# Kernel optimization log

Measured on AMD Instinct MI355X. Metric: run time of the kernel, lower is better.

## Reference

```python
import jax, jax.numpy as jnp
import numpy as np

EMBED_DIM = 1024
NUM_HEADS = 16
HEAD_DIM = EMBED_DIM // NUM_HEADS
SCALE = HEAD_DIM ** -0.5


def setup_inputs() -> dict:
    key = jax.random.key(0)
    ks = jax.random.split(key, 5)
    B, S = 4, 2048
    x = jax.random.normal(ks[0], (B, S, EMBED_DIM), dtype=jnp.float32)
    # Dense(embed_dim*3): kernel [D, 3D], bias [3D] (Keras glorot_uniform; use scaled normal)
    w_qkv = jax.random.normal(ks[1], (EMBED_DIM, 3 * EMBED_DIM), dtype=jnp.float32) * (1.0 / np.sqrt(EMBED_DIM))
    b_qkv = jnp.zeros((3 * EMBED_DIM,), dtype=jnp.float32)
    w_proj = jax.random.normal(ks[2], (EMBED_DIM, EMBED_DIM), dtype=jnp.float32) * (1.0 / np.sqrt(EMBED_DIM))
    b_proj = jnp.zeros((EMBED_DIM,), dtype=jnp.float32)
    return {"x": x, "w_qkv": w_qkv, "b_qkv": b_qkv, "w_proj": w_proj, "b_proj": b_proj}


def reference(x, w_qkv, b_qkv, w_proj, b_proj):
    B, S, D = x.shape
    qkv = x @ w_qkv + b_qkv
    qkv = qkv.reshape(B, S, 3, NUM_HEADS, HEAD_DIM)
    qkv = jnp.transpose(qkv, (2, 0, 3, 1, 4))
    q, k, v = qkv[0], qkv[1], qkv[2]
    # scaled dot-product attention (full [B,H,S,S] scores, matching source)
    attn_logits = jnp.einsum('bhqd,bhkd->bhqk', q, k) * SCALE
    attn = jax.nn.softmax(attn_logits, axis=-1)
    context = jnp.einsum('bhqk,bhkd->bhqd', attn, v)
    context = jnp.transpose(context, (0, 2, 1, 3)).reshape(B, S, D)
    out = context @ w_proj + b_proj
    return out
```

## Files before the change

### kernel.cpp

```cpp
#include <hip/hip_runtime.h>

typedef unsigned short u16;
typedef __attribute__((ext_vector_type(8))) short bf16x8;
typedef __attribute__((ext_vector_type(4))) float f32x4;
typedef __attribute__((ext_vector_type(16))) float f32x16;

__device__ __forceinline__ float bf2f(u16 x) {
  union { unsigned u; float f; } v; v.u = ((unsigned)x) << 16; return v.f;
}
__device__ __forceinline__ u16 f2bf(float f) {
  union { float f; unsigned u; } v; v.f = f;
  unsigned r = v.u + 0x7FFFu + ((v.u >> 16) & 1u);
  return (u16)(r >> 16);
}
__device__ __forceinline__ float clampf(float v) {
  return fmaxf(fminf(v, 1.0e4f), -1.0e4f);
}
__device__ __forceinline__ void gll16(const u16* g, u16* l) {
  __builtin_amdgcn_global_load_lds(
      (const __attribute__((address_space(1))) void*)g,
      (__attribute__((address_space(3))) void*)l, 16, 0, 0);
}
__device__ __forceinline__ unsigned cvtpk(float lo, float hi) {
  unsigned r;
  asm("v_cvt_pk_bf16_f32 %0, %1, %2" : "=v"(r) : "v"(lo), "v"(hi));
  return r;
}

__global__ __launch_bounds__(256) void convert_x(
    const float* __restrict__ x, u16* __restrict__ xbf) {
  const int i0 = (blockIdx.x * 256 + threadIdx.x) * 4;
  const float4 v = *(const float4*)(x + i0);
  xbf[i0 + 0] = f2bf(v.x); xbf[i0 + 1] = f2bf(v.y);
  xbf[i0 + 2] = f2bf(v.z); xbf[i0 + 3] = f2bf(v.w);
}

__global__ __launch_bounds__(256) void transpose_f32_bf16(
    const float* __restrict__ in, u16* __restrict__ out, int R, int C) {
  __shared__ u16 tile[32][33];
  const int bc = blockIdx.x * 32, br = blockIdx.y * 32;
  const int tx = threadIdx.x & 31, ty = threadIdx.x >> 5;
  #pragma unroll
  for (int i = ty; i < 32; i += 8)
    tile[i][tx] = f2bf(in[(size_t)(br + i) * C + bc + tx]);
  __syncthreads();
  #pragma unroll
  for (int i = ty; i < 32; i += 8)
    out[(size_t)(bc + i) * R + br + tx] = tile[tx][i];
}

__global__ __launch_bounds__(256) void gemm1_qkv(
    const u16* __restrict__ A, const u16* __restrict__ Bt,
    const float* __restrict__ bias, u16* __restrict__ qk,
    u16* __restrict__ vt, int K) {
  __shared__ u16 As0[128 * 32], As1[128 * 32];
  __shared__ u16 Bs0[128 * 32], Bs1[128 * 32];
  const int tid = threadIdx.x;
  const int m0 = blockIdx.x * 128, n0 = blockIdx.y * 128;
  const int wave = tid >> 6, lane = tid & 63;
  const int quad = lane >> 4, l16 = lane & 15;
  const int wm = (wave >> 1) * 64, wn = (wave & 1) * 64;
  const int sr = (lane >> 2), sp = lane & 3;

  f32x4 acc[4][4] = {};
  const u16* gA = A + (size_t)(m0 + wave * 32 + sr) * K + sp * 8;
  const u16* gB = Bt + (size_t)(n0 + wave * 32 + sr) * K + sp * 8;

  for (int k0 = 0; k0 < K; k0 += 64) {
    #pragma unroll
    for (int t = 0; t < 2; ++t) {
      gll16(gA + (size_t)(t * 16) * K + k0,      &As0[(wave * 32 + t * 16) * 32]);
      gll16(gA + (size_t)(t * 16) * K + k0 + 32, &As1[(wave * 32 + t * 16) * 32]);
      gll16(gB + (size_t)(t * 16) * K + k0,      &Bs0[(wave * 32 + t * 16) * 32]);
      gll16(gB + (size_t)(t * 16) * K + k0 + 32, &Bs1[(wave * 32 + t * 16) * 32]);
    }
    __syncthreads();
    #pragma unroll
    for (int ks = 0; ks < 2; ++ks) {
      const u16* Ah = ks ? As1 : As0;
      const u16* Bh = ks ? Bs1 : Bs0;
      bf16x8 af[4], bfr[4];
      #pragma unroll
      for (int i = 0; i < 4; ++i)
        af[i] = *(const bf16x8*)&Ah[(wm + i * 16 + l16) * 32 + quad * 8];
      #pragma unroll
      for (int j = 0; j < 4; ++j)
        bfr[j] = *(const bf16x8*)&Bh[(wn + j * 16 + l16) * 32 + quad * 8];
      #pragma unroll
      for (int i = 0; i < 4; ++i)
        #pragma unroll
        for (int j = 0; j < 4; ++j)
          acc[i][j] = __builtin_amdgcn_mfma_f32_16x16x32_bf16(af[i], bfr[j], acc[i][j], 0, 0, 0);
    }
    __syncthreads();
  }

  #pragma unroll
  for (int i = 0; i < 4; ++i) {
    const int row = m0 + wm + i * 16 + quad * 4;
    #pragma unroll
    for (int j = 0; j < 4; ++j) {
      const int col = n0 + wn + j * 16 + l16;
      const float bv = bias[col];
      if (col < 2048) {
        #pragma unroll
        for (int r = 0; r < 4; ++r)
          qk[(size_t)(row + r) * 2048 + col] = f2bf(clampf(acc[i][j][r] + bv));
      } else {
        const int d = col & 63;
        const int hh = (col - 2048) >> 6;
        #pragma unroll
        for (int r = 0; r < 4; ++r) {
          const int rr = row + r;
          const int bb = rr >> 11, ss = rr & 2047;
          vt[(size_t)(bb * 16 + hh) * 131072 + d * 2048 + ss] =
              f2bf(clampf(acc[i][j][r] + bv));
        }
      }
    }
  }
}

__global__ __launch_bounds__(256) void gemm2_proj(
    const u16* __restrict__ A, const u16* __restrict__ Bt,
    const float* __restrict__ bias, float* __restrict__ out, int K) {
  __shared__ u16 As0[128 * 32], As1[128 * 32];
  __shared__ u16 Bs0[128 * 32], Bs1[128 * 32];
  const int tid = threadIdx.x;
  const int m0 = blockIdx.x * 128, n0 = blockIdx.y * 128;
  const int wave = tid >> 6, lane = tid & 63;
  const int quad = lane >> 4, l16 = lane & 15;
  const int wm = (wave >> 1) * 64, wn = (wave & 1) * 64;
  const int sr = (lane >> 2), sp = lane & 3;

  f32x4 acc[4][4] = {};
  const u16* gA = A + (size_t)(m0 + wave * 32 + sr) * K + sp * 8;
  const u16* gB = Bt + (size_t)(n0 + wave * 32 + sr) * K + sp * 8;

  for (int k0 = 0; k0 < K; k0 += 64) {
    #pragma unroll
    for (int t = 0; t < 2; ++t) {
      gll16(gA + (size_t)(t * 16) * K + k0,      &As0[(wave * 32 + t * 16) * 32]);
      gll16(gA + (size_t)(t * 16) * K + k0 + 32, &As1[(wave * 32 + t * 16) * 32]);
      gll16(gB + (size_t)(t * 16) * K + k0,      &Bs0[(wave * 32 + t * 16) * 32]);
      gll16(gB + (size_t)(t * 16) * K + k0 + 32, &Bs1[(wave * 32 + t * 16) * 32]);
    }
    __syncthreads();
    #pragma unroll
    for (int ks = 0; ks < 2; ++ks) {
      const u16* Ah = ks ? As1 : As0;
      const u16* Bh = ks ? Bs1 : Bs0;
      bf16x8 af[4], bfr[4];
      #pragma unroll
      for (int i = 0; i < 4; ++i)
        af[i] = *(const bf16x8*)&Ah[(wm + i * 16 + l16) * 32 + quad * 8];
      #pragma unroll
      for (int j = 0; j < 4; ++j)
        bfr[j] = *(const bf16x8*)&Bh[(wn + j * 16 + l16) * 32 + quad * 8];
      #pragma unroll
      for (int i = 0; i < 4; ++i)
        #pragma unroll
        for (int j = 0; j < 4; ++j)
          acc[i][j] = __builtin_amdgcn_mfma_f32_16x16x32_bf16(af[i], bfr[j], acc[i][j], 0, 0, 0);
    }
    __syncthreads();
  }

  #pragma unroll
  for (int i = 0; i < 4; ++i) {
    const int row = m0 + wm + i * 16 + quad * 4;
    #pragma unroll
    for (int j = 0; j < 4; ++j) {
      const int col = n0 + wn + j * 16 + l16;
      const float bv = bias[col];
      #pragma unroll
      for (int r = 0; r < 4; ++r)
        out[(size_t)(row + r) * 1024 + col] = clampf(acc[i][j][r] + bv);
    }
  }
}

__device__ __forceinline__ int swz(int row, int col) {
  const int key = (row ^ (row >> 2)) & 7;
  return row * 64 + (((col >> 3) ^ key) << 3) + (col & 7);
}

__global__ __launch_bounds__(256, 4) void attn_fused(
    const u16* __restrict__ qk, const u16* __restrict__ vt,
    u16* __restrict__ ctx) {
  __shared__ u16 Ks[64 * 64];
  __shared__ u16 VsT[64 * 64];
  __shared__ u16 big[10240];
  const int bh = blockIdx.x, qt = blockIdx.y;
  const int b = bh >> 4, h = bh & 15;
  const int tid = threadIdx.x;
  const int w = tid >> 6, lane = tid & 63;
  const int l31 = lane & 31, hl = lane >> 5;
  const int qbase = qt * 128 + w * 32;
  const int xaddr = (lane ^ 32) << 2;

  const u16* qptr = qk + (size_t)(b * 2048) * 2048 + h * 64;
  bf16x8 qf[4];
  #pragma unroll
  for (int ds = 0; ds < 4; ++ds)
    qf[ds] = *(const bf16x8*)(qptr + (size_t)(qbase + l31) * 2048 + ds * 16 + hl * 8);

  const u16* kptr = qk + (size_t)(b * 2048) * 2048 + 1024 + h * 64;
  const u16* vptr = vt + (size_t)bh * 131072;

  const int srow = tid >> 3, scol = (tid & 7) * 8;

  const int st0 = swz(srow, scol);
  const int st1 = swz(srow + 32, scol);
  int off[2][4];
  #pragma unroll
  for (int a = 0; a < 2; ++a)
    #pragma unroll
    for (int d = 0; d < 4; ++d)
      off[a][d] = swz(a * 32 + l31, d * 16 + hl * 8);

  const u16* kB0 = kptr + (size_t)srow * 2048 + scol;
  const u16* kB1 = kptr + (size_t)(srow + 32) * 2048 + scol;
  const u16* vB0 = vptr + (size_t)srow * 2048 + scol;
  const u16* vB1 = vptr + (size_t)(srow + 32) * 2048 + scol;

  f32x16 o[2] = {};
  float lacc = 0.0f;
  const float c2 = 0.125f * 1.44269504088896340736f;

  bf16x8 k0 = *(const bf16x8*)kB0;
  bf16x8 k1 = *(const bf16x8*)kB1;
  bf16x8 v0 = *(const bf16x8*)vB0;
  bf16x8 v1 = *(const bf16x8*)vB1;

  for (int kv0 = 0; kv0 < 2048; kv0 += 64) {
    __syncthreads();
    *(bf16x8*)&Ks[st0]  = k0;
    *(bf16x8*)&Ks[st1]  = k1;
    *(bf16x8*)&VsT[st0] = v0;
    *(bf16x8*)&VsT[st1] = v1;
    __syncthreads();
    const int kvn = (kv0 + 64) & 2047;
    k0 = *(const bf16x8*)(kB0 + (size_t)kvn * 2048);
    k1 = *(const bf16x8*)(kB1 + (size_t)kvn * 2048);
    v0 = *(const bf16x8*)(vB0 + kvn);
    v1 = *(const bf16x8*)(vB1 + kvn);

    #pragma unroll
    for (int kb = 0; kb < 2; ++kb) {
      f32x16 s = {};
      #pragma unroll
      for (int ds = 0; ds < 4; ++ds) {
        bf16x8 kf = *(const bf16x8*)&Ks[off[kb][ds]];
        s = __builtin_amdgcn_mfma_f32_32x32x16_bf16(kf, qf[ds], s, 0, 0, 0);
      }
      #pragma unroll
      for (int r = 0; r < 16; ++r)
        s[r] = __builtin_amdgcn_exp2f(s[r] * c2);
      {
        float t0 = (s[0] + s[1]) + (s[2] + s[3]);
        float t1 = (s[4] + s[5]) + (s[6] + s[7]);
        float t2 = (s[8] + s[9]) + (s[10] + s[11]);
        float t3 = (s[12] + s[13]) + (s[14] + s[15]);
        lacc += (t0 + t1) + (t2 + t3);
      }
      #pragma unroll
      for (int ksl = 0; ksl < 2; ++ksl) {
        const int r0 = ksl * 8;
        unsigned cA = cvtpk(s[r0 + 0], s[r0 + 1]);
        unsigned cB = cvtpk(s[r0 + 2], s[r0 + 3]);
        unsigned cC = cvtpk(s[r0 + 4], s[r0 + 5]);
        unsigned cD = cvtpk(s[r0 + 6], s[r0 + 7]);
        const unsigned bA = (unsigned)__builtin_amdgcn_ds_bpermute(xaddr, (int)cA);
        const unsigned bB = (unsigned)__builtin_amdgcn_ds_bpermute(xaddr, (int)cB);
        const unsigned bC = (unsigned)__builtin_amdgcn_ds_bpermute(xaddr, (int)cC);
        const unsigned bD = (unsigned)__builtin_amdgcn_ds_bpermute(xaddr, (int)cD);
        union { unsigned u[4]; bf16x8 v; } pf;
        pf.u[0] = hl ? bC : cA;
        pf.u[1] = hl ? bD : cB;
        pf.u[2] = hl ? cC : bA;
        pf.u[3] = hl ? cD : bB;
        const int kg = kb * 2 + ksl;
        #pragma unroll
        for (int db = 0; db < 2; ++db) {
          bf16x8 vf = *(const bf16x8*)&VsT[off[db][kg]];
          o[db] = __builtin_amdgcn_mfma_f32_32x32x16_bf16(pf.v, vf, o[db], 0, 0, 0);
        }
      }
    }
  }

  {
    union { float f; int i; } a, rr;
    a.f = lacc;
    rr.i = __builtin_amdgcn_ds_bpermute(xaddr, a.i);
    lacc = lacc + rr.f;
  }
  float* dnm = (float*)big;
  if (lane < 32) dnm[w * 32 + lane] = lacc;
  u16* cbase = ctx + (size_t)(b * 2048) * 1024 + h * 64;
  #pragma unroll
  for (int r = 0; r < 16; ++r) {
    const int q0 = (r & 3) + 8 * (r >> 2) + 4 * hl;
    const float inv = 1.0f / dnm[w * 32 + q0];
    const size_t qrow = (size_t)(qbase + q0);
    cbase[qrow * 1024 + l31]      = f2bf(o[0][r] * inv);
    cbase[qrow * 1024 + 32 + l31] = f2bf(o[1][r] * inv);
  }
}

extern "C" void kernel_launch(void* const* d_in, const int* in_sizes, int n_in,
                              void* d_out, int out_size, void* d_ws, size_t ws_size,
                              hipStream_t stream) {
  (void)out_size;
  const float *x = nullptr, *wq = nullptr, *bq = nullptr, *wp = nullptr, *bp = nullptr;
  for (int i = 0; i < n_in; ++i) {
    switch (in_sizes[i]) {
      case 8388608: x  = (const float*)d_in[i]; break;
      case 3145728: wq = (const float*)d_in[i]; break;
      case 3072:    bq = (const float*)d_in[i]; break;
      case 1048576: wp = (const float*)d_in[i]; break;
      case 1024:    bp = (const float*)d_in[i]; break;
      default: break;
    }
  }
  if (!x || !wq || !bq || !wp || !bp) {
    x  = (const float*)d_in[0]; wq = (const float*)d_in[1];
    bq = (const float*)d_in[2]; wp = (const float*)d_in[3];
    bp = (const float*)d_in[4];
  }
  float* out = (float*)d_out;

  const size_t NEED = 75497472;
  if (ws_size < NEED) return;

  char* ws = (char*)d_ws;
  u16* qkb = (u16*)(ws);
  u16* vt  = (u16*)(ws + 33554432);
  u16* xbf = (u16*)(ws + 50331648);
  u16* wT1 = (u16*)(ws + 67108864);
  u16* wT2 = (u16*)(ws + 73400320);

  convert_x<<<8192, 256, 0, stream>>>(x, xbf);
  transpose_f32_bf16<<<dim3(96, 32), 256, 0, stream>>>(wq, wT1, 1024, 3072);
  transpose_f32_bf16<<<dim3(32, 32), 256, 0, stream>>>(wp, wT2, 1024, 1024);
  gemm1_qkv<<<dim3(64, 24), 256, 0, stream>>>(xbf, wT1, bq, qkb, vt, 1024);
  attn_fused<<<dim3(64, 16), 256, 0, stream>>>(qkb, vt, xbf );
  gemm2_proj<<<dim3(64, 8), 256, 0, stream>>>(xbf , wT2, bp, out, 1024);
}
```

Measured before the change: 280.5 us.

## Compute softmax row sums via MFMA with ones and use permlane32 swap

Instead of summing exp values on VALU and exchanging them with ds_bpermute, each P tile is multiplied by an all-ones bf16 operand through an extra MFMA, so the row sums land in the accumulator layout that matches the output. The cross-half lane exchange of packed P values switches from four ds_bpermute calls plus selects to two v_permlane32_swap instructions. s_setprio is raised around the MFMA groups to favour matrix issue. Costs are one extra MFMA per 32x16 slice, plus row sums now taken from bf16-rounded P rather than fp32 values, which slightly changes the normalization.

```diff
diff --git a/kernel.cpp b/kernel.cpp
--- a/kernel.cpp
+++ b/kernel.cpp
@@ -197,7 +197,6 @@
   const int w = tid >> 6, lane = tid & 63;
   const int l31 = lane & 31, hl = lane >> 5;
   const int qbase = qt * 128 + w * 32;
-  const int xaddr = (lane ^ 32) << 2;
 
   const u16* qptr = qk + (size_t)(b * 2048) * 2048 + h * 64;
   bf16x8 qf[4];
@@ -225,7 +224,9 @@
   const u16* vB1 = vptr + (size_t)(srow + 32) * 2048 + scol;
 
   f32x16 o[2] = {};
-  float lacc = 0.0f;
+  f32x16 lsum = {};
+  const short one = (short)0x3F80;
+  const bf16x8 ones = {one, one, one, one, one, one, one, one};
   const float c2 = 0.125f * 1.44269504088896340736f;
 
   bf16x8 k0 = *(const bf16x8*)kB0;
@@ -249,21 +250,16 @@
     #pragma unroll
     for (int kb = 0; kb < 2; ++kb) {
       f32x16 s = {};
+      __builtin_amdgcn_s_setprio(1);
       #pragma unroll
       for (int ds = 0; ds < 4; ++ds) {
         bf16x8 kf = *(const bf16x8*)&Ks[off[kb][ds]];
         s = __builtin_amdgcn_mfma_f32_32x32x16_bf16(kf, qf[ds], s, 0, 0, 0);
       }
+      __builtin_amdgcn_s_setprio(0);
       #pragma unroll
       for (int r = 0; r < 16; ++r)
         s[r] = __builtin_amdgcn_exp2f(s[r] * c2);
-      {
-        float t0 = (s[0] + s[1]) + (s[2] + s[3]);
-        float t1 = (s[4] + s[5]) + (s[6] + s[7]);
-        float t2 = (s[8] + s[9]) + (s[10] + s[11]);
-        float t3 = (s[12] + s[13]) + (s[14] + s[15]);
-        lacc += (t0 + t1) + (t2 + t3);
-      }
       #pragma unroll
       for (int ksl = 0; ksl < 2; ++ksl) {
         const int r0 = ksl * 8;
@@ -271,38 +267,33 @@
         unsigned cB = cvtpk(s[r0 + 2], s[r0 + 3]);
         unsigned cC = cvtpk(s[r0 + 4], s[r0 + 5]);
         unsigned cD = cvtpk(s[r0 + 6], s[r0 + 7]);
-        const unsigned bA = (unsigned)__builtin_amdgcn_ds_bpermute(xaddr, (int)cA);
-        const unsigned bB = (unsigned)__builtin_amdgcn_ds_bpermute(xaddr, (int)cB);
-        const unsigned bC = (unsigned)__builtin_amdgcn_ds_bpermute(xaddr, (int)cC);
-        const unsigned bD = (unsigned)__builtin_amdgcn_ds_bpermute(xaddr, (int)cD);
+        asm volatile("v_permlane32_swap_b32 %0, %1" : "+v"(cA), "+v"(cC));
+        asm volatile("v_permlane32_swap_b32 %0, %1" : "+v"(cB), "+v"(cD));
         union { unsigned u[4]; bf16x8 v; } pf;
-        pf.u[0] = hl ? bC : cA;
-        pf.u[1] = hl ? bD : cB;
-        pf.u[2] = hl ? cC : bA;
-        pf.u[3] = hl ? cD : bB;
+        pf.u[0] = cA;
+        pf.u[1] = cB;
+        pf.u[2] = cC;
+        pf.u[3] = cD;
         const int kg = kb * 2 + ksl;
+        __builtin_amdgcn_s_setprio(1);
+        lsum = __builtin_amdgcn_mfma_f32_32x32x16_bf16(pf.v, ones, lsum, 0, 0, 0);
         #pragma unroll
         for (int db = 0; db < 2; ++db) {
           bf16x8 vf = *(const bf16x8*)&VsT[off[db][kg]];
           o[db] = __builtin_amdgcn_mfma_f32_32x32x16_bf16(pf.v, vf, o[db], 0, 0, 0);
         }
+        __builtin_amdgcn_s_setprio(0);
       }
     }
   }
 
-  {
-    union { float f; int i; } a, rr;
-    a.f = lacc;
-    rr.i = __builtin_amdgcn_ds_bpermute(xaddr, a.i);
-    lacc = lacc + rr.f;
-  }
-  float* dnm = (float*)big;
-  if (lane < 32) dnm[w * 32 + lane] = lacc;
+  if (lane < 32) ((float*)big)[w * 32 + lane] = lsum[0];
+
   u16* cbase = ctx + (size_t)(b * 2048) * 1024 + h * 64;
   #pragma unroll
   for (int r = 0; r < 16; ++r) {
     const int q0 = (r & 3) + 8 * (r >> 2) + 4 * hl;
-    const float inv = 1.0f / dnm[w * 32 + q0];
+    const float inv = 1.0f / lsum[r];
     const size_t qrow = (size_t)(qbase + q0);
     cbase[qrow * 1024 + l31]      = f2bf(o[0][r] * inv);
     cbase[qrow * 1024 + 32 + l31] = f2bf(o[1][r] * inv);
```

New measurement: 282.1 us. No clear change (+0.6%).
